# Performance work log

Hardware: AMD Instinct MI355X
Metric: run time of the kernel (lower is better)

Reference implementation:

```python
import jax, jax.numpy as jnp
import numpy as np

N = 50000      # nodes
E = 800000     # edges
D = 256        # embed_dim
H = 8          # num_heads
HD = D // H    # head_dim = 32
F = 4 * D      # feedforward_dim = 1024
SCALE = D ** -0.5  # note: module scales by embed_dim**-0.5, not head_dim
EPS = 1e-5


def setup_inputs() -> dict:
    key = jax.random.key(0)
    ks = jax.random.split(key, 10)
    x = jax.random.normal(ks[0], (N, D), dtype=jnp.float32)
    edge_indices = jax.random.randint(ks[1], (2, E), 0, N, dtype=jnp.int32)
    s = 0.02
    return {
        "x": x,
        "edge_indices": edge_indices,
        "w_qkv": jax.random.normal(ks[2], (D, 3 * D), dtype=jnp.float32) * s,
        "b_qkv": jnp.zeros((3 * D,), dtype=jnp.float32),
        "ln1_g": jnp.ones((D,), dtype=jnp.float32),
        "ln1_b": jnp.zeros((D,), dtype=jnp.float32),
        "ln2_g": jnp.ones((D,), dtype=jnp.float32),
        "ln2_b": jnp.zeros((D,), dtype=jnp.float32),
        "w1": jax.random.normal(ks[3], (D, F), dtype=jnp.float32) * s,
        "b1": jnp.zeros((F,), dtype=jnp.float32),
        "w2": jax.random.normal(ks[4], (F, D), dtype=jnp.float32) * s,
        "b2": jnp.zeros((D,), dtype=jnp.float32),
    }


def _layer_norm(x, g, b):
    m = jnp.mean(x, axis=-1, keepdims=True)
    v = jnp.mean((x - m) ** 2, axis=-1, keepdims=True)
    return (x - m) * jax.lax.rsqrt(v + EPS) * g + b


def _self_attention(x, edge_indices, w_qkv, b_qkv):
    qkv = (x @ w_qkv + b_qkv).reshape(N, H, 3 * HD)
    q, k, v = qkv[..., :HD], qkv[..., HD:2 * HD], qkv[..., 2 * HD:]
    rows, cols = edge_indices[0], edge_indices[1]
    # per-edge, per-head attention logits: [E, H]
    alpha = jnp.einsum('ehd,ehd->eh', q[rows], k[cols]) * SCALE
    # sparse softmax over each row (destination node) segment
    m = jax.ops.segment_max(alpha, rows, num_segments=N)       # [N, H]
    ea = jnp.exp(alpha - m[rows])                              # [E, H]
    denom = jax.ops.segment_sum(ea, rows, num_segments=N)      # [N, H]
    w = ea / denom[rows]                                       # [E, H]
    # per-head SpMM: out[r] += w_e * v[c]  -> [N, H, HD]
    out = jax.ops.segment_sum(w[:, :, None] * v[cols], rows, num_segments=N)
    return out.reshape(N, D)


def reference(x, edge_indices, w_qkv, b_qkv, ln1_g, ln1_b, ln2_g, ln2_b, w1, b1, w2, b2):
    # post-norm (norm_first=False), dropout=0
    x = _layer_norm(x + _self_attention(x, edge_indices, w_qkv, b_qkv), ln1_g, ln1_b)
    ffn = jax.nn.relu(x @ w1 + b1) @ w2 + b2
    x = _layer_norm(x + ffn, ln2_g, ln2_b)
    return x
```

## Files before the change

### kernel.cpp

```cpp
#include <hip/hip_runtime.h>
#include <hip/hip_bf16.h>

#define N_NODES 50000
#define E_EDGES 800000
#define D_MODEL 256
#define H_HEADS 8
#define HDIM    32
#define F_FFN   1024
#define ATT_SCALE 0.0625f
#define LN_EPS  1e-5f
#define NB_SCAN 196

typedef __attribute__((ext_vector_type(8))) short bf16x8;
typedef __attribute__((ext_vector_type(4))) float f32x4;

__device__ __forceinline__ float bf2f(__hip_bfloat16 v) { return __bfloat162float(v); }
__device__ __forceinline__ __hip_bfloat16 f2bf(float v) { return __float2bfloat16(v); }
__device__ __forceinline__ unsigned short bfbits(float f) {
    __hip_bfloat16 h = __float2bfloat16(f);
    return *reinterpret_cast<unsigned short*>(&h);
}

__device__ __forceinline__ float4 load_bf16x4(const __hip_bfloat16* p) {
    uint2 u = *reinterpret_cast<const uint2*>(p);
    float4 r;
    r.x = __uint_as_float(u.x << 16);
    r.y = __uint_as_float(u.x & 0xFFFF0000u);
    r.z = __uint_as_float(u.y << 16);
    r.w = __uint_as_float(u.y & 0xFFFF0000u);
    return r;
}

__device__ __forceinline__ void load_lds16(const void* g, void* l) {
    __builtin_amdgcn_global_load_lds(
        (const __attribute__((address_space(1))) unsigned*)g,
        (__attribute__((address_space(3))) unsigned*)l, 16, 0, 0);
}


#define PREP_X   3200000
#define PREP_WQ  (768 * 256)
#define PREP_W1  (1024 * 256)
#define PREP_W2  (256 * 1024)
#define PREP_BQ  768
#define PREP_B1  1024
#define PREP_TOT (PREP_X + PREP_WQ + PREP_W1 + PREP_W2 + PREP_BQ + PREP_B1 + N_NODES)
__global__ void prep_kernel(const float* __restrict__ x, unsigned short* __restrict__ xb,
                            const float* __restrict__ wq, __hip_bfloat16* __restrict__ wtq,
                            const float* __restrict__ w1, __hip_bfloat16* __restrict__ wt1,
                            const float* __restrict__ w2, __hip_bfloat16* __restrict__ wt2,
                            const float* __restrict__ bq, float* __restrict__ bqp,
                            const float* __restrict__ b1, float* __restrict__ b1p,
                            unsigned* __restrict__ counts, unsigned* __restrict__ cursor) {
    int i = blockIdx.x * blockDim.x + threadIdx.x;
    if (i < PREP_X) {
        float4 v = reinterpret_cast<const float4*>(x)[i];
        ushort4 o;
        o.x = bfbits(v.x); o.y = bfbits(v.y); o.z = bfbits(v.z); o.w = bfbits(v.w);
        reinterpret_cast<ushort4*>(xb)[i] = o;
        return;
    }
    i -= PREP_X;
    if (i < PREP_WQ) {
        int n = i >> 8, k = i & 255;
        int s = n >> 8, prel = n & 255;
        int d = (prel & 192) + ((prel & 15) << 2) + ((prel >> 4) & 3);
        int co = (d >> 5) * 96 + s * 32 + (d & 31);
        wtq[i] = f2bf(wq[(size_t)k * 768 + co]);
        return;
    }
    i -= PREP_WQ;
    if (i < PREP_W1) {
        int n = i >> 8, k = i & 255;
        int f = (n & ~63) + ((n & 15) << 2) + ((n >> 4) & 3);
        wt1[i] = f2bf(w1[(size_t)k * 1024 + f]);
        return;
    }
    i -= PREP_W1;
    if (i < PREP_W2) {
        int n = i >> 10, k = i & 1023;
        wt2[i] = f2bf(w2[(size_t)k * 256 + n]);
        return;
    }
    i -= PREP_W2;
    if (i < PREP_BQ) {
        int s = i >> 8, prel = i & 255;
        int d = (prel & 192) + ((prel & 15) << 2) + ((prel >> 4) & 3);
        bqp[i] = bq[(d >> 5) * 96 + s * 32 + (d & 31)];
        return;
    }
    i -= PREP_BQ;
    if (i < PREP_B1) {
        int f = (i & ~63) + ((i & 15) << 2) + ((i >> 4) & 3);
        b1p[i] = b1[f];
        return;
    }
    i -= PREP_B1;
    if (i < N_NODES) { counts[i] = 0u; cursor[i] = 0u; }
}

template<bool RELU, int EPI>
__global__ __launch_bounds__(256)
void mfma_gemm(const __hip_bfloat16* __restrict__ A,
               const __hip_bfloat16* __restrict__ Wt,
               const float* __restrict__ bias,
               __hip_bfloat16* __restrict__ outp,
               __hip_bfloat16* __restrict__ qb,
               unsigned char* __restrict__ kv8,
               int M, int Ncols, int K) {
    __shared__ short Al[128 * 32];
    __shared__ short Bl[128 * 32];
    const int t = threadIdx.x;
    const int wave = t >> 6, lane = t & 63;

    unsigned flat = blockIdx.y * gridDim.x + blockIdx.x;
    unsigned nwg = gridDim.x * gridDim.y;
    unsigned q8 = nwg >> 3, r8 = nwg & 7;
    unsigned xcd = flat & 7, pos = flat >> 3;
    unsigned wg = (xcd < r8) ? (xcd * (q8 + 1) + pos)
                             : (r8 * (q8 + 1) + (xcd - r8) * q8 + pos);
    const int m0 = (int)(wg / gridDim.x) * 128;
    const int n0 = (int)(wg % gridDim.x) * 128;

    const int wr = wave >> 1, wc = wave & 1;

    const int srow = lane >> 2;
    const int skp  = (lane & 3) ^ ((lane >> 3) & 3);
    const int c0 = wave * 2;
    int ar0 = m0 + c0 * 16 + srow;      if (ar0 >= M) ar0 = M - 1;
    int ar1 = m0 + c0 * 16 + 16 + srow; if (ar1 >= M) ar1 = M - 1;
    const __hip_bfloat16* ga0 = A + (size_t)ar0 * K + skp * 8;
    const __hip_bfloat16* ga1 = A + (size_t)ar1 * K + skp * 8;
    const __hip_bfloat16* gb0 = Wt + (size_t)(n0 + c0 * 16 + srow) * K + skp * 8;
    const __hip_bfloat16* gb1 = Wt + (size_t)(n0 + c0 * 16 + 16 + srow) * K + skp * 8;
    short* la0 = &Al[c0 * 512];
    short* la1 = &Al[c0 * 512 + 512];
    short* lb0 = &Bl[c0 * 512];
    short* lb1 = &Bl[c0 * 512 + 512];

    const int lh = lane & 15, q = lane >> 4;
    const int qs = q ^ ((lane >> 1) & 3);
    const short* fa = &Al[(wr * 64 + lh) * 32 + qs * 8];
    const short* fb = &Bl[(wc * 64 + lh) * 32 + qs * 8];

    f32x4 acc[4][4] = {};

    for (int k0 = 0; k0 < K; k0 += 32) {
        load_lds16(ga0, la0);
        load_lds16(ga1, la1);
        load_lds16(gb0, lb0);
        load_lds16(gb1, lb1);
        ga0 += 32; ga1 += 32; gb0 += 32; gb1 += 32;
        __syncthreads();

        bf16x8 af[4], bfr[4];
#pragma unroll
        for (int i = 0; i < 4; i++) {
            af[i]  = *reinterpret_cast<const bf16x8*>(fa + i * 16 * 32);
            bfr[i] = *reinterpret_cast<const bf16x8*>(fb + i * 16 * 32);
        }
#pragma unroll
        for (int mi = 0; mi < 4; mi++)
#pragma unroll
            for (int nj = 0; nj < 4; nj++)
                acc[mi][nj] = __builtin_amdgcn_mfma_f32_16x16x32_bf16(
                    af[mi], bfr[nj], acc[mi][nj], 0, 0, 0);
        __syncthreads();
    }

    const int B = n0 + wc * 64;
    const int gnbase = B + lh;
    float bv[4];
#pragma unroll
    for (int nj = 0; nj < 4; nj++) bv[nj] = bias[gnbase + nj * 16];

    if (EPI == 0) {
        const int sec = B >> 8;
        const int c = ((B & 255) >> 6) * 16 + lh;
#pragma unroll
        for (int mi = 0; mi < 4; mi++) {
            int gmb = m0 + wr * 64 + mi * 16 + q * 4;
#pragma unroll
            for (int r = 0; r < 4; r++) {
                int gm = gmb + r;
                if (gm >= M) continue;
                float v0 = acc[mi][0][r] + bv[0];
                float v1 = acc[mi][1][r] + bv[1];
                float v2 = acc[mi][2][r] + bv[2];
                float v3 = acc[mi][3][r] + bv[3];
                if (sec == 0) {
                    ushort4 o;
                    o.x = bfbits(v0); o.y = bfbits(v1); o.z = bfbits(v2); o.w = bfbits(v3);
                    *reinterpret_cast<ushort4*>(qb + (size_t)gm * 256 + c * 4) = o;
                } else {
                    unsigned u = (unsigned)__builtin_amdgcn_cvt_pk_fp8_f32(v0, v1, 0, false);
                    u = (unsigned)__builtin_amdgcn_cvt_pk_fp8_f32(v2, v3, (int)u, true);
                    *reinterpret_cast<unsigned*>(
                        kv8 + (size_t)gm * 512 + c * 8 + (sec == 1 ? 0 : 4)) = u;
                }
            }
        }
    } else {
        const int cb = B + lh * 4;
#pragma unroll
        for (int mi = 0; mi < 4; mi++) {
            int gmb = m0 + wr * 64 + mi * 16 + q * 4;
#pragma unroll
            for (int r = 0; r < 4; r++) {
                int gm = gmb + r;
                if (gm >= M) continue;
                float v0 = acc[mi][0][r] + bv[0];
                float v1 = acc[mi][1][r] + bv[1];
                float v2 = acc[mi][2][r] + bv[2];
                float v3 = acc[mi][3][r] + bv[3];
                if (RELU) {
                    v0 = fmaxf(v0, 0.f); v1 = fmaxf(v1, 0.f);
                    v2 = fmaxf(v2, 0.f); v3 = fmaxf(v3, 0.f);
                }
                ushort4 o;
                o.x = bfbits(v0); o.y = bfbits(v1); o.z = bfbits(v2); o.w = bfbits(v3);
                *reinterpret_cast<ushort4*>(outp + (size_t)gm * Ncols + cb) = o;
            }
        }
    }
}

__global__ __launch_bounds__(512)
void ffn2_ln_kernel(const __hip_bfloat16* __restrict__ A,
                    const __hip_bfloat16* __restrict__ Wt,
                    const float* __restrict__ bias,
                    const __hip_bfloat16* __restrict__ resid,
                    const float* __restrict__ g, const float* __restrict__ bb,
                    float* __restrict__ out, int M) {
    __shared__ short LDS[2][(64 + 256) * 32];
    const int t = threadIdx.x;
    const int wave = t >> 6, lane = t & 63;
    const int m0 = blockIdx.x * 64;
    const int wr = wave >> 2, wc = wave & 3;

    const int srow = lane >> 2;
    const int skp  = (lane & 3) ^ ((lane >> 3) & 3);

    const __hip_bfloat16* gsrc0; int loff0;
    const __hip_bfloat16* gsrc1; int loff1;
    const __hip_bfloat16* gsrc2; int loff2;
    {
#define STAGE_INIT(GS, LO, C)                                            \
        if ((C) < 4) {                                                   \
            int r_ = m0 + (C) * 16 + srow; if (r_ >= M) r_ = M - 1;      \
            GS = A + (size_t)r_ * 1024 + skp * 8;                        \
            LO = (C) * 512;                                              \
        } else {                                                         \
            GS = Wt + (size_t)(((C) - 4) * 16 + srow) * 1024 + skp * 8;  \
            LO = 2048 + ((C) - 4) * 512;                                 \
        }
        STAGE_INIT(gsrc0, loff0, wave)
        STAGE_INIT(gsrc1, loff1, wave + 8)
        int c2 = (wave < 4) ? wave + 16 : 16;
        STAGE_INIT(gsrc2, loff2, c2)
#undef STAGE_INIT
    }

    const int lh = lane & 15, q = lane >> 4;
    const int qs = q ^ ((lane >> 1) & 3);
    const short* fa0 = &LDS[0][(wr * 32 + lh) * 32 + qs * 8];
    const short* fb0 = &LDS[0][2048 + (wc * 64 + lh) * 32 + qs * 8];
    const short* fa1 = &LDS[1][(wr * 32 + lh) * 32 + qs * 8];
    const short* fb1 = &LDS[1][2048 + (wc * 64 + lh) * 32 + qs * 8];

    f32x4 acc[2][4] = {};

#define FFN2_STAGE(BUF)                                      \
    load_lds16(gsrc0, &LDS[BUF][loff0]);                     \
    load_lds16(gsrc1, &LDS[BUF][loff1]);                     \
    if (wave < 4) load_lds16(gsrc2, &LDS[BUF][loff2]);       \
    gsrc0 += 32; gsrc1 += 32; gsrc2 += 32;

#define FFN2_STEP(FA, FB)                                                   \
    {                                                                       \
        bf16x8 af[2], bfr[4];                                               \
        _Pragma("unroll")                                                   \
        for (int i = 0; i < 2; i++)                                         \
            af[i] = *reinterpret_cast<const bf16x8*>((FA) + i * 16 * 32);   \
        _Pragma("unroll")                                                   \
        for (int i = 0; i < 4; i++)                                         \
            bfr[i] = *reinterpret_cast<const bf16x8*>((FB) + i * 16 * 32);  \
        _Pragma("unroll")                                                   \
        for (int mi = 0; mi < 2; mi++)                                      \
            _Pragma("unroll")                                               \
            for (int nj = 0; nj < 4; nj++)                                  \
                acc[mi][nj] = __builtin_amdgcn_mfma_f32_16x16x32_bf16(      \
                    af[mi], bfr[nj], acc[mi][nj], 0, 0, 0);                 \
    }

    FFN2_STAGE(0)
    __syncthreads();

    for (int s = 0; s < 32; s += 2) {
        FFN2_STAGE(1)
        FFN2_STEP(fa0, fb0)
        __syncthreads();
        if (s < 30) { FFN2_STAGE(0) }
        FFN2_STEP(fa1, fb1)
        __syncthreads();
    }
#undef FFN2_STAGE
#undef FFN2_STEP

    const int colbase = wc * 64 + lh;
    float bv[4], gv[4], bbv[4];
#pragma unroll
    for (int nj = 0; nj < 4; nj++) {
        bv[nj]  = bias[colbase + nj * 16];
        gv[nj]  = g[colbase + nj * 16];
        bbv[nj] = bb[colbase + nj * 16];
    }

    float ps[2][4], pq[2][4];
#pragma unroll
    for (int mi = 0; mi < 2; mi++) {
#pragma unroll
        for (int r = 0; r < 4; r++) {
            int gm = m0 + wr * 32 + mi * 16 + q * 4 + r;
            int rgm = (gm < M) ? gm : M - 1;
            float s = 0.f, s2 = 0.f;
#pragma unroll
            for (int nj = 0; nj < 4; nj++) {
                float v = acc[mi][nj][r] + bv[nj]
                        + bf2f(resid[(size_t)rgm * 256 + colbase + nj * 16]);
                acc[mi][nj][r] = v;
                s += v; s2 += v * v;
            }
            ps[mi][r] = s; pq[mi][r] = s2;
        }
    }
#pragma unroll
    for (int off = 1; off <= 8; off <<= 1) {
#pragma unroll
        for (int mi = 0; mi < 2; mi++)
#pragma unroll
            for (int r = 0; r < 4; r++) {
                ps[mi][r] += __shfl_xor(ps[mi][r], off);
                pq[mi][r] += __shfl_xor(pq[mi][r], off);
            }
    }
    float* rs = (float*)(&LDS[0][0]);
    float* rq = rs + 256;
    if (lh == 0) {
#pragma unroll
        for (int mi = 0; mi < 2; mi++)
#pragma unroll
            for (int r = 0; r < 4; r++) {
                int m = wr * 32 + mi * 16 + q * 4 + r;
                rs[m * 4 + wc] = ps[mi][r];
                rq[m * 4 + wc] = pq[mi][r];
            }
    }
    __syncthreads();

#pragma unroll
    for (int mi = 0; mi < 2; mi++) {
#pragma unroll
        for (int r = 0; r < 4; r++) {
            int m = wr * 32 + mi * 16 + q * 4 + r;
            int gm = m0 + m;
            if (gm >= M) continue;
            float4 rsv = *reinterpret_cast<const float4*>(&rs[m * 4]);
            float4 rqv = *reinterpret_cast<const float4*>(&rq[m * 4]);
            float S  = (rsv.x + rsv.y) + (rsv.z + rsv.w);
            float S2 = (rqv.x + rqv.y) + (rqv.z + rqv.w);
            float mean = S * (1.f / (float)D_MODEL);
            float var  = S2 * (1.f / (float)D_MODEL) - mean * mean;
            float inv  = rsqrtf(var + LN_EPS);
#pragma unroll
            for (int nj = 0; nj < 4; nj++)
                out[(size_t)gm * 256 + colbase + nj * 16] =
                    (acc[mi][nj][r] - mean) * inv * gv[nj] + bbv[nj];
        }
    }
}

__global__ void count_kernel(const int* __restrict__ rows, unsigned* __restrict__ counts) {
    int e = blockIdx.x * blockDim.x + threadIdx.x;
    if (e < E_EDGES) atomicAdd(&counts[rows[e]], 1u);
}

__global__ void scan_blk_kernel(const unsigned* __restrict__ counts,
                                unsigned* __restrict__ offs, unsigned* __restrict__ bsum) {
    __shared__ unsigned sh[256];
    int t = threadIdx.x;
    int i = blockIdx.x * 256 + t;
    unsigned v = (i < N_NODES) ? counts[i] : 0u;
    sh[t] = v;
    __syncthreads();
#pragma unroll
    for (int off = 1; off < 256; off <<= 1) {
        unsigned u = (t >= off) ? sh[t - off] : 0u;
        __syncthreads();
        sh[t] += u;
        __syncthreads();
    }
    if (i < N_NODES) offs[i] = sh[t] - v;
    if (t == 255) bsum[blockIdx.x] = sh[255];
}

__global__ void scan_top_kernel(const unsigned* __restrict__ bsum, unsigned* __restrict__ bpre) {
    __shared__ unsigned sh[256];
    int t = threadIdx.x;
    unsigned v = (t < NB_SCAN) ? bsum[t] : 0u;
    sh[t] = v;
    __syncthreads();
#pragma unroll
    for (int off = 1; off < 256; off <<= 1) {
        unsigned u = (t >= off) ? sh[t - off] : 0u;
        __syncthreads();
        sh[t] += u;
        __syncthreads();
    }
    if (t < NB_SCAN) bpre[t] = sh[t] - v;
    if (t == NB_SCAN - 1) bpre[NB_SCAN] = sh[t];
}

__global__ void scan_add_kernel(unsigned* __restrict__ offs, const unsigned* __restrict__ bpre) {
    int i = blockIdx.x * 256 + threadIdx.x;
    if (i < N_NODES) offs[i] += bpre[blockIdx.x];
    if (i == 0) offs[N_NODES] = bpre[NB_SCAN];
}

__global__ void scatter_kernel(const int* __restrict__ rows, const int* __restrict__ cols,
                               const unsigned* __restrict__ offsets, unsigned* __restrict__ cursor,
                               int* __restrict__ scol) {
    int e = blockIdx.x * blockDim.x + threadIdx.x;
    if (e >= E_EDGES) return;
    int r = rows[e];
    unsigned idx = atomicAdd(&cursor[r], 1u);
    scol[offsets[r] + idx] = cols[e];
}

__global__ __launch_bounds__(256)
void att_agg_kernel(const __hip_bfloat16* __restrict__ qb,
                    const unsigned char* __restrict__ kv8,
                    const unsigned* __restrict__ offsets,
                    const int* __restrict__ scol,
                    const float* __restrict__ x,
                    const float* __restrict__ g, const float* __restrict__ bb,
                    __hip_bfloat16* __restrict__ xn) {
    int n = blockIdx.x * 4 + (threadIdx.x >> 6);
    if (n >= N_NODES) return;
    int lam = threadIdx.x & 63;
    unsigned beg = offsets[n], end = offsets[n + 1];

    float4 qf = load_bf16x4(qb + (size_t)n * 256 + lam * 4);
    qf.x *= ATT_SCALE; qf.y *= ATT_SCALE; qf.z *= ATT_SCALE; qf.w *= ATT_SCALE;

    float4 acc = {0.f, 0.f, 0.f, 0.f};
    float l = 0.f;

#define EDGE_BODY(KV, SV, PV)                                                 \
    unsigned klo = (unsigned)(KV), vhi = (unsigned)((KV) >> 32);              \
    auto k01 = __builtin_amdgcn_cvt_pk_f32_fp8((int)klo, false);              \
    auto k23 = __builtin_amdgcn_cvt_pk_f32_fp8((int)klo, true);               \
    float SV = qf.x * k01[0] + qf.y * k01[1] + qf.z * k23[0] + qf.w * k23[1]; \
    SV += __shfl_xor(SV, 1);                                                  \
    SV += __shfl_xor(SV, 2);                                                  \
    SV += __shfl_xor(SV, 4);                                                  \
    float PV = __expf(SV);                                                    \
    auto v01 = __builtin_amdgcn_cvt_pk_f32_fp8((int)vhi, false);              \
    auto v23 = __builtin_amdgcn_cvt_pk_f32_fp8((int)vhi, true);               \
    l += PV;                                                                  \
    acc.x += PV * v01[0]; acc.y += PV * v01[1];                               \
    acc.z += PV * v23[0]; acc.w += PV * v23[1];

    unsigned e = beg;
    for (; e + 4 <= end; e += 4) {
        int c0 = scol[e], c1 = scol[e + 1], c2 = scol[e + 2], c3 = scol[e + 3];
        unsigned long long kv0 = *(const unsigned long long*)(kv8 + (size_t)c0 * 512 + lam * 8);
        unsigned long long kv1 = *(const unsigned long long*)(kv8 + (size_t)c1 * 512 + lam * 8);
        unsigned long long kv2 = *(const unsigned long long*)(kv8 + (size_t)c2 * 512 + lam * 8);
        unsigned long long kv3 = *(const unsigned long long*)(kv8 + (size_t)c3 * 512 + lam * 8);
        { EDGE_BODY(kv0, s0, p0) }
        { EDGE_BODY(kv1, s1, p1) }
        { EDGE_BODY(kv2, s2, p2) }
        { EDGE_BODY(kv3, s3, p3) }
    }
    for (; e < end; e++) {
        int c0 = scol[e];
        unsigned long long kv0 = *(const unsigned long long*)(kv8 + (size_t)c0 * 512 + lam * 8);
        { EDGE_BODY(kv0, s0, p0) }
    }
#undef EDGE_BODY

    float inv_l = (l > 0.f) ? 1.f / l : 0.f;
    float4 xr = reinterpret_cast<const float4*>(x + (size_t)n * D_MODEL)[lam];
    float4 tv;
    tv.x = acc.x * inv_l + xr.x;
    tv.y = acc.y * inv_l + xr.y;
    tv.z = acc.z * inv_l + xr.z;
    tv.w = acc.w * inv_l + xr.w;

    float s  = tv.x + tv.y + tv.z + tv.w;
    float s2 = tv.x * tv.x + tv.y * tv.y + tv.z * tv.z + tv.w * tv.w;
#pragma unroll
    for (int off = 1; off <= 32; off <<= 1) {
        s  += __shfl_xor(s, off);
        s2 += __shfl_xor(s2, off);
    }
    float mean = s * (1.f / (float)D_MODEL);
    float var  = s2 * (1.f / (float)D_MODEL) - mean * mean;
    float inv  = rsqrtf(var + LN_EPS);

    float4 gr = reinterpret_cast<const float4*>(g  + lam * 4)[0];
    float4 br = reinterpret_cast<const float4*>(bb + lam * 4)[0];
    ushort4 o;
    o.x = bfbits((tv.x - mean) * inv * gr.x + br.x);
    o.y = bfbits((tv.y - mean) * inv * gr.y + br.y);
    o.z = bfbits((tv.z - mean) * inv * gr.z + br.z);
    o.w = bfbits((tv.w - mean) * inv * gr.w + br.w);
    reinterpret_cast<ushort4*>(xn + (size_t)n * D_MODEL)[lam] = o;
}

extern "C" void kernel_launch(void* const* d_in, const int* in_sizes, int n_in,
                              void* d_out, int out_size, void* d_ws, size_t ws_size,
                              hipStream_t stream) {
    const float* x     = (const float*)d_in[0];
    const int*   ei    = (const int*)d_in[1];
    const float* w_qkv = (const float*)d_in[2];
    const float* b_qkv = (const float*)d_in[3];
    const float* ln1_g = (const float*)d_in[4];
    const float* ln1_b = (const float*)d_in[5];
    const float* ln2_g = (const float*)d_in[6];
    const float* ln2_b = (const float*)d_in[7];
    const float* w1    = (const float*)d_in[8];
    const float* b1    = (const float*)d_in[9];
    const float* w2    = (const float*)d_in[10];
    const float* b2    = (const float*)d_in[11];
    const int* rows = ei;
    const int* cols = ei + E_EDGES;

    char* ws = (char*)d_ws;
    __hip_bfloat16* qb      = (__hip_bfloat16*)(ws + 0);
    unsigned char*  kv8     = (unsigned char*)(ws + 25600000);
    __hip_bfloat16* hbuf    = (__hip_bfloat16*)(ws + 0);
    __hip_bfloat16* xb      = (__hip_bfloat16*)(ws + 102400000);
    __hip_bfloat16* wtq     = (__hip_bfloat16*)(ws + 128000000);
    __hip_bfloat16* wt1     = (__hip_bfloat16*)(ws + 128400000);
    __hip_bfloat16* wt2     = (__hip_bfloat16*)(ws + 129000000);
    unsigned*       counts  = (unsigned*)(ws + 129600000);
    unsigned*       offsets = (unsigned*)(ws + 129800000);
    unsigned*       cursor  = (unsigned*)(ws + 130000008);
    int*            scol    = (int*)(ws + 130200008);
    unsigned*       bsum    = (unsigned*)(ws + 133400008);
    unsigned*       bpre    = (unsigned*)(ws + 133401032);
    float*          bqp     = (float*)(ws + 133500000);
    float*          b1p     = (float*)(ws + 133510000);
    __hip_bfloat16* xn      = (__hip_bfloat16*)(ws + 153600000);

    const int nbM = (N_NODES + 127) / 128;

    prep_kernel<<<(PREP_TOT + 255) / 256, 256, 0, stream>>>(
        x, (unsigned short*)xb, w_qkv, wtq, w1, wt1, w2, wt2,
        b_qkv, bqp, b1, b1p, counts, cursor);

    mfma_gemm<false, 0><<<dim3(768 / 128, nbM), 256, 0, stream>>>(
        xb, wtq, bqp, nullptr, qb, kv8, N_NODES, 768, D_MODEL);

    count_kernel<<<(E_EDGES + 255) / 256, 256, 0, stream>>>(rows, counts);
    scan_blk_kernel<<<NB_SCAN, 256, 0, stream>>>(counts, offsets, bsum);
    scan_top_kernel<<<1, 256, 0, stream>>>(bsum, bpre);
    scan_add_kernel<<<NB_SCAN, 256, 0, stream>>>(offsets, bpre);
    scatter_kernel<<<(E_EDGES + 255) / 256, 256, 0, stream>>>(rows, cols, offsets, cursor, scol);

    att_agg_kernel<<<(N_NODES + 3) / 4, 256, 0, stream>>>(qb, kv8, offsets, scol,
                                                          x, ln1_g, ln1_b, xn);

    mfma_gemm<true, 1><<<dim3(F_FFN / 128, nbM), 256, 0, stream>>>(
        xn, wt1, b1p, hbuf, nullptr, nullptr, N_NODES, F_FFN, D_MODEL);

    ffn2_ln_kernel<<<(N_NODES + 63) / 64, 512, 0, stream>>>(hbuf, wt2, b2, xn, ln2_g, ln2_b,
                                                            (float*)d_out, N_NODES);
}
```

Baseline: 426.5 us.

## Double-buffer GEMM LDS tiles and process two edges per wave in attention

```diff
diff --git a/kernel.cpp b/kernel.cpp
--- a/kernel.cpp
+++ b/kernel.cpp
@@ -12,6 +12,7 @@
 #define NB_SCAN 196
 
 typedef __attribute__((ext_vector_type(8))) short bf16x8;
+typedef __attribute__((ext_vector_type(8))) unsigned short u16x8;
 typedef __attribute__((ext_vector_type(4))) float f32x4;
 
 __device__ __forceinline__ float bf2f(__hip_bfloat16 v) { return __bfloat162float(v); }
@@ -21,14 +22,11 @@
     return *reinterpret_cast<unsigned short*>(&h);
 }
 
-__device__ __forceinline__ float4 load_bf16x4(const __hip_bfloat16* p) {
-    uint2 u = *reinterpret_cast<const uint2*>(p);
-    float4 r;
-    r.x = __uint_as_float(u.x << 16);
-    r.y = __uint_as_float(u.x & 0xFFFF0000u);
-    r.z = __uint_as_float(u.y << 16);
-    r.w = __uint_as_float(u.y & 0xFFFF0000u);
-    return r;
+__device__ __forceinline__ void unpack_bf8(uint4 u, float* f) {
+    f[0] = __uint_as_float(u.x << 16); f[1] = __uint_as_float(u.x & 0xFFFF0000u);
+    f[2] = __uint_as_float(u.y << 16); f[3] = __uint_as_float(u.y & 0xFFFF0000u);
+    f[4] = __uint_as_float(u.z << 16); f[5] = __uint_as_float(u.z & 0xFFFF0000u);
+    f[6] = __uint_as_float(u.w << 16); f[7] = __uint_as_float(u.w & 0xFFFF0000u);
 }
 
 __device__ __forceinline__ void load_lds16(const void* g, void* l) {
@@ -108,8 +106,8 @@
                __hip_bfloat16* __restrict__ qb,
                unsigned char* __restrict__ kv8,
                int M, int Ncols, int K) {
-    __shared__ short Al[128 * 32];
-    __shared__ short Bl[128 * 32];
+    __shared__ short Al[2][128 * 32];
+    __shared__ short Bl[2][128 * 32];
     const int t = threadIdx.x;
     const int wave = t >> 6, lane = t & 63;
 
@@ -133,40 +131,52 @@
     const __hip_bfloat16* ga1 = A + (size_t)ar1 * K + skp * 8;
     const __hip_bfloat16* gb0 = Wt + (size_t)(n0 + c0 * 16 + srow) * K + skp * 8;
     const __hip_bfloat16* gb1 = Wt + (size_t)(n0 + c0 * 16 + 16 + srow) * K + skp * 8;
-    short* la0 = &Al[c0 * 512];
-    short* la1 = &Al[c0 * 512 + 512];
-    short* lb0 = &Bl[c0 * 512];
-    short* lb1 = &Bl[c0 * 512 + 512];
 
     const int lh = lane & 15, q = lane >> 4;
     const int qs = q ^ ((lane >> 1) & 3);
-    const short* fa = &Al[(wr * 64 + lh) * 32 + qs * 8];
-    const short* fb = &Bl[(wc * 64 + lh) * 32 + qs * 8];
+    const short* fa0 = &Al[0][(wr * 64 + lh) * 32 + qs * 8];
+    const short* fb0 = &Bl[0][(wc * 64 + lh) * 32 + qs * 8];
+    const short* fa1 = &Al[1][(wr * 64 + lh) * 32 + qs * 8];
+    const short* fb1 = &Bl[1][(wc * 64 + lh) * 32 + qs * 8];
 
     f32x4 acc[4][4] = {};
 
-    for (int k0 = 0; k0 < K; k0 += 32) {
-        load_lds16(ga0, la0);
-        load_lds16(ga1, la1);
-        load_lds16(gb0, lb0);
-        load_lds16(gb1, lb1);
-        ga0 += 32; ga1 += 32; gb0 += 32; gb1 += 32;
-        __syncthreads();
-
-        bf16x8 af[4], bfr[4];
-#pragma unroll
-        for (int i = 0; i < 4; i++) {
-            af[i]  = *reinterpret_cast<const bf16x8*>(fa + i * 16 * 32);
-            bfr[i] = *reinterpret_cast<const bf16x8*>(fb + i * 16 * 32);
-        }
-#pragma unroll
-        for (int mi = 0; mi < 4; mi++)
-#pragma unroll
-            for (int nj = 0; nj < 4; nj++)
-                acc[mi][nj] = __builtin_amdgcn_mfma_f32_16x16x32_bf16(
-                    af[mi], bfr[nj], acc[mi][nj], 0, 0, 0);
-        __syncthreads();
-    }
+#define GSTAGE(B)                                    \
+    load_lds16(ga0, &Al[B][c0 * 512]);               \
+    load_lds16(ga1, &Al[B][c0 * 512 + 512]);         \
+    load_lds16(gb0, &Bl[B][c0 * 512]);               \
+    load_lds16(gb1, &Bl[B][c0 * 512 + 512]);         \
+    ga0 += 32; ga1 += 32; gb0 += 32; gb1 += 32;
+
+#define GSTEP(FA, FB)                                                       \
+    {                                                                       \
+        bf16x8 af[4], bfr[4];                                               \
+        _Pragma("unroll")                                                   \
+        for (int i = 0; i < 4; i++) {                                       \
+            af[i]  = *reinterpret_cast<const bf16x8*>((FA) + i * 16 * 32);  \
+            bfr[i] = *reinterpret_cast<const bf16x8*>((FB) + i * 16 * 32);  \
+        }                                                                   \
+        _Pragma("unroll")                                                   \
+        for (int mi = 0; mi < 4; mi++)                                      \
+            _Pragma("unroll")                                               \
+            for (int nj = 0; nj < 4; nj++)                                  \
+                acc[mi][nj] = __builtin_amdgcn_mfma_f32_16x16x32_bf16(      \
+                    af[mi], bfr[nj], acc[mi][nj], 0, 0, 0);                 \
+    }
+
+    const int nsteps = K >> 5;
+    GSTAGE(0)
+    __syncthreads();
+    for (int s = 0; s < nsteps; s += 2) {
+        if (s + 1 < nsteps) { GSTAGE(1) }
+        GSTEP(fa0, fb0)
+        __syncthreads();
+        if (s + 2 < nsteps) { GSTAGE(0) }
+        GSTEP(fa1, fb1)
+        __syncthreads();
+    }
+#undef GSTAGE
+#undef GSTEP
 
     const int B = n0 + wc * 64;
     const int gnbase = B + lh;
@@ -447,61 +457,88 @@
                     __hip_bfloat16* __restrict__ xn) {
     int n = blockIdx.x * 4 + (threadIdx.x >> 6);
     if (n >= N_NODES) return;
-    int lam = threadIdx.x & 63;
+    const int lam = threadIdx.x & 63;
+    const int hl  = lam & 31;
+    const int sel = lam >> 5;
     unsigned beg = offsets[n], end = offsets[n + 1];
 
-    float4 qf = load_bf16x4(qb + (size_t)n * 256 + lam * 4);
-    qf.x *= ATT_SCALE; qf.y *= ATT_SCALE; qf.z *= ATT_SCALE; qf.w *= ATT_SCALE;
-
-    float4 acc = {0.f, 0.f, 0.f, 0.f};
+    float qv[8];
+    {
+        uint4 u = *reinterpret_cast<const uint4*>(qb + (size_t)n * 256 + hl * 8);
+        unpack_bf8(u, qv);
+#pragma unroll
+        for (int i = 0; i < 8; i++) qv[i] *= ATT_SCALE;
+    }
+
+    float acc[8] = {};
     float l = 0.f;
 
-#define EDGE_BODY(KV, SV, PV)                                                 \
-    unsigned klo = (unsigned)(KV), vhi = (unsigned)((KV) >> 32);              \
-    auto k01 = __builtin_amdgcn_cvt_pk_f32_fp8((int)klo, false);              \
-    auto k23 = __builtin_amdgcn_cvt_pk_f32_fp8((int)klo, true);               \
-    float SV = qf.x * k01[0] + qf.y * k01[1] + qf.z * k23[0] + qf.w * k23[1]; \
-    SV += __shfl_xor(SV, 1);                                                  \
-    SV += __shfl_xor(SV, 2);                                                  \
-    SV += __shfl_xor(SV, 4);                                                  \
-    float PV = __expf(SV);                                                    \
-    auto v01 = __builtin_amdgcn_cvt_pk_f32_fp8((int)vhi, false);              \
-    auto v23 = __builtin_amdgcn_cvt_pk_f32_fp8((int)vhi, true);               \
-    l += PV;                                                                  \
-    acc.x += PV * v01[0]; acc.y += PV * v01[1];                               \
-    acc.z += PV * v23[0]; acc.w += PV * v23[1];
+#define PAIR_BODY(W, VMUL)                                                      \
+    {                                                                           \
+        auto k01 = __builtin_amdgcn_cvt_pk_f32_fp8((int)(W).x, false);          \
+        auto k23 = __builtin_amdgcn_cvt_pk_f32_fp8((int)(W).x, true);           \
+        auto k45 = __builtin_amdgcn_cvt_pk_f32_fp8((int)(W).z, false);          \
+        auto k67 = __builtin_amdgcn_cvt_pk_f32_fp8((int)(W).z, true);           \
+        float sv = qv[0] * k01[0] + qv[1] * k01[1] + qv[2] * k23[0]             \
+                 + qv[3] * k23[1] + qv[4] * k45[0] + qv[5] * k45[1]             \
+                 + qv[6] * k67[0] + qv[7] * k67[1];                             \
+        sv += __shfl_xor(sv, 1);                                                \
+        sv += __shfl_xor(sv, 2);                                                \
+        float pv = __expf(sv) * (VMUL);                                         \
+        l += pv;                                                                \
+        auto v01 = __builtin_amdgcn_cvt_pk_f32_fp8((int)(W).y, false);          \
+        auto v23 = __builtin_amdgcn_cvt_pk_f32_fp8((int)(W).y, true);           \
+        auto v45 = __builtin_amdgcn_cvt_pk_f32_fp8((int)(W).w, false);          \
+        auto v67 = __builtin_amdgcn_cvt_pk_f32_fp8((int)(W).w, true);           \
+        acc[0] += pv * v01[0]; acc[1] += pv * v01[1];                           \
+        acc[2] += pv * v23[0]; acc[3] += pv * v23[1];                           \
+        acc[4] += pv * v45[0]; acc[5] += pv * v45[1];                           \
+        acc[6] += pv * v67[0]; acc[7] += pv * v67[1];                           \
+    }
 
     unsigned e = beg;
     for (; e + 4 <= end; e += 4) {
-        int c0 = scol[e], c1 = scol[e + 1], c2 = scol[e + 2], c3 = scol[e + 3];
-        unsigned long long kv0 = *(const unsigned long long*)(kv8 + (size_t)c0 * 512 + lam * 8);
-        unsigned long long kv1 = *(const unsigned long long*)(kv8 + (size_t)c1 * 512 + lam * 8);
-        unsigned long long kv2 = *(const unsigned long long*)(kv8 + (size_t)c2 * 512 + lam * 8);
-        unsigned long long kv3 = *(const unsigned long long*)(kv8 + (size_t)c3 * 512 + lam * 8);
-        { EDGE_BODY(kv0, s0, p0) }
-        { EDGE_BODY(kv1, s1, p1) }
-        { EDGE_BODY(kv2, s2, p2) }
-        { EDGE_BODY(kv3, s3, p3) }
-    }
-    for (; e < end; e++) {
-        int c0 = scol[e];
-        unsigned long long kv0 = *(const unsigned long long*)(kv8 + (size_t)c0 * 512 + lam * 8);
-        { EDGE_BODY(kv0, s0, p0) }
-    }
-#undef EDGE_BODY
+        int cA = scol[e + sel];
+        int cB = scol[e + 2 + sel];
+        uint4 wa = *reinterpret_cast<const uint4*>(kv8 + (size_t)cA * 512 + hl * 16);
+        uint4 wb = *reinterpret_cast<const uint4*>(kv8 + (size_t)cB * 512 + hl * 16);
+        PAIR_BODY(wa, 1.0f)
+        PAIR_BODY(wb, 1.0f)
+    }
+    if (e + 2 <= end) {
+        int cA = scol[e + sel];
+        uint4 wa = *reinterpret_cast<const uint4*>(kv8 + (size_t)cA * 512 + hl * 16);
+        PAIR_BODY(wa, 1.0f)
+        e += 2;
+    }
+    if (e < end) {
+        int cA = scol[e];
+        uint4 wa = *reinterpret_cast<const uint4*>(kv8 + (size_t)cA * 512 + hl * 16);
+        PAIR_BODY(wa, sel ? 0.0f : 1.0f)
+    }
+#undef PAIR_BODY
+
+    l += __shfl_xor(l, 32);
+#pragma unroll
+    for (int i = 0; i < 8; i++) acc[i] += __shfl_xor(acc[i], 32);
 
     float inv_l = (l > 0.f) ? 1.f / l : 0.f;
-    float4 xr = reinterpret_cast<const float4*>(x + (size_t)n * D_MODEL)[lam];
-    float4 tv;
-    tv.x = acc.x * inv_l + xr.x;
-    tv.y = acc.y * inv_l + xr.y;
-    tv.z = acc.z * inv_l + xr.z;
-    tv.w = acc.w * inv_l + xr.w;
-
-    float s  = tv.x + tv.y + tv.z + tv.w;
-    float s2 = tv.x * tv.x + tv.y * tv.y + tv.z * tv.z + tv.w * tv.w;
-#pragma unroll
-    for (int off = 1; off <= 32; off <<= 1) {
+
+    float tv[8];
+    {
+        const float4* xr = reinterpret_cast<const float4*>(x + (size_t)n * D_MODEL);
+        float4 x0 = xr[hl * 2], x1 = xr[hl * 2 + 1];
+        tv[0] = acc[0] * inv_l + x0.x; tv[1] = acc[1] * inv_l + x0.y;
+        tv[2] = acc[2] * inv_l + x0.z; tv[3] = acc[3] * inv_l + x0.w;
+        tv[4] = acc[4] * inv_l + x1.x; tv[5] = acc[5] * inv_l + x1.y;
+        tv[6] = acc[6] * inv_l + x1.z; tv[7] = acc[7] * inv_l + x1.w;
+    }
+
+    float s = 0.f, s2 = 0.f;
+#pragma unroll
+    for (int i = 0; i < 8; i++) { s += tv[i]; s2 += tv[i] * tv[i]; }
+#pragma unroll
+    for (int off = 1; off <= 16; off <<= 1) {
         s  += __shfl_xor(s, off);
         s2 += __shfl_xor(s2, off);
     }
@@ -509,14 +546,19 @@
     float var  = s2 * (1.f / (float)D_MODEL) - mean * mean;
     float inv  = rsqrtf(var + LN_EPS);
 
-    float4 gr = reinterpret_cast<const float4*>(g  + lam * 4)[0];
-    float4 br = reinterpret_cast<const float4*>(bb + lam * 4)[0];
-    ushort4 o;
-    o.x = bfbits((tv.x - mean) * inv * gr.x + br.x);
-    o.y = bfbits((tv.y - mean) * inv * gr.y + br.y);
-    o.z = bfbits((tv.z - mean) * inv * gr.z + br.z);
-    o.w = bfbits((tv.w - mean) * inv * gr.w + br.w);
-    reinterpret_cast<ushort4*>(xn + (size_t)n * D_MODEL)[lam] = o;
+    if (sel == 0) {
+        const float4* gp = reinterpret_cast<const float4*>(g);
+        const float4* bp = reinterpret_cast<const float4*>(bb);
+        float4 g0 = gp[hl * 2], g1 = gp[hl * 2 + 1];
+        float4 b0 = bp[hl * 2], b1 = bp[hl * 2 + 1];
+        float gv[8] = {g0.x, g0.y, g0.z, g0.w, g1.x, g1.y, g1.z, g1.w};
+        float bv[8] = {b0.x, b0.y, b0.z, b0.w, b1.x, b1.y, b1.z, b1.w};
+        u16x8 o;
+#pragma unroll
+        for (int i = 0; i < 8; i++)
+            o[i] = bfbits((tv[i] - mean) * inv * gv[i] + bv[i]);
+        *reinterpret_cast<u16x8*>(xn + (size_t)n * D_MODEL + hl * 8) = o;
+    }
 }
 
 extern "C" void kernel_launch(void* const* d_in, const int* in_sizes, int n_in,
```

After: 415.6 us. 1.03x faster.
